# Optimization experiments

Measured on AMD Instinct MI355X. Metric: run time of the kernel, lower is better.

## Reference

```python
import jax, jax.numpy as jnp
import numpy as np

D_MODEL = 512
D_STATE = 16
D_CONV = 4
D_INNER = 2 * D_MODEL          # expand = 2 (mamba_ssm default)
DT_RANK = (D_MODEL + 15) // 16  # ceil(d_model/16) = 32
B, L = 2, 2048


def setup_inputs() -> dict:
    key = jax.random.key(0)
    ks = jax.random.split(key, 12)
    s = lambda k, shp, sc: jax.random.normal(k, shp, jnp.float32) * sc
    return {
        "x": s(ks[0], (B, L, D_MODEL), 1.0),
        "context": s(ks[1], (B, L, D_MODEL), 1.0),
        # Mamba params
        "in_proj_w": s(ks[2], (2 * D_INNER, D_MODEL), 0.02),
        "conv_w": s(ks[3], (D_INNER, D_CONV), 0.2),        # depthwise conv kernel
        "conv_b": jnp.zeros((D_INNER,), jnp.float32),
        "x_proj_w": s(ks[4], (DT_RANK + 2 * D_STATE, D_INNER), 0.02),
        "dt_proj_w": s(ks[5], (D_INNER, DT_RANK), 0.1),
        "dt_proj_b": s(ks[6], (D_INNER,), 0.1),
        "A_log": jnp.log(jnp.tile(jnp.arange(1, D_STATE + 1, dtype=jnp.float32), (D_INNER, 1))),
        "D": jnp.ones((D_INNER,), jnp.float32),
        "out_proj_w": s(ks[7], (D_MODEL, D_INNER), 0.02),
        # context gate params
        "gate_w": s(ks[8], (D_MODEL, 2 * D_MODEL), 0.02),
        "gate_b": jnp.zeros((D_MODEL,), jnp.float32),
    }


def _mamba(x, in_proj_w, conv_w, conv_b, x_proj_w, dt_proj_w, dt_proj_b, A_log, D, out_proj_w):
    Bsz, Ln, _ = x.shape
    # input projection -> [B, L, 2*E], split into ssm branch xi and gate z
    xz = jnp.einsum('bld,ed->ble', x, in_proj_w)
    xi, z = jnp.split(xz, 2, axis=-1)
    # causal depthwise conv1d (kernel D_CONV) + SiLU
    xp = jnp.pad(xi, ((0, 0), (D_CONV - 1, 0), (0, 0)))
    xc = sum(xp[:, k:k + Ln, :] * conv_w[:, k] for k in range(D_CONV)) + conv_b
    xc = jax.nn.silu(xc)
    # input-dependent dt, B, C
    dbc = jnp.einsum('ble,fe->blf', xc, x_proj_w)
    dt, Bm, Cm = jnp.split(dbc, [DT_RANK, DT_RANK + D_STATE], axis=-1)
    dt = jax.nn.softplus(jnp.einsum('blr,er->ble', dt, dt_proj_w) + dt_proj_b)  # [B,L,E]
    A = -jnp.exp(A_log)                                   # [E,S]
    dA = jnp.exp(dt[..., None] * A)                       # [B,L,E,S]
    dBx = dt[..., None] * Bm[:, :, None, :] * xc[..., None]  # [B,L,E,S]

    def step(h, ins):
        dA_t, dBx_t, C_t = ins
        h = dA_t * h + dBx_t                              # [B,E,S]
        y = jnp.einsum('bes,bs->be', h, C_t)
        return h, y

    h0 = jnp.zeros((Bsz, D_INNER, D_STATE), x.dtype)
    _, ys = jax.lax.scan(step, h0,
                         (dA.transpose(1, 0, 2, 3), dBx.transpose(1, 0, 2, 3), Cm.transpose(1, 0, 2)))
    y = ys.transpose(1, 0, 2) + xc * D                    # skip term D*x
    y = y * jax.nn.silu(z)                                # gated output
    return jnp.einsum('ble,de->bld', y, out_proj_w)


def reference(x, context, in_proj_w, conv_w, conv_b, x_proj_w, dt_proj_w, dt_proj_b,
              A_log, D, out_proj_w, gate_w, gate_b):
    m = _mamba(x, in_proj_w, conv_w, conv_b, x_proj_w, dt_proj_w, dt_proj_b, A_log, D, out_proj_w)
    g_in = jnp.concatenate([m, context], axis=-1)         # [B,L,2*d_model]
    gate = jax.nn.sigmoid(jnp.einsum('ble,de->bld', g_in, gate_w) + gate_b)
    return m * gate
```

## Files before the change

kernel.cpp:

```cpp
#include <hip/hip_runtime.h>
#include <cstdint>
#include <cstddef>

#define B_SZ   2
#define L_SZ   2048
#define BL     (B_SZ * L_SZ)
#define DMODEL 512
#define DINNER 1024
#define DSTATE 16
#define DTRANK 32
#define DTROWS 16
#define NCH    32
#define CHL    (L_SZ / NCH)

typedef unsigned short u16;
typedef __attribute__((ext_vector_type(8))) short          bf16x8;
typedef __attribute__((ext_vector_type(8))) unsigned short u16x8;
typedef __attribute__((ext_vector_type(4))) float          f32x4;

__device__ __forceinline__ void gload16(const void* g, void* l) {
    __builtin_amdgcn_global_load_lds(
        (const __attribute__((address_space(1))) unsigned int*)g,
        (__attribute__((address_space(3))) unsigned int*)l, 16, 0, 0);
}

__device__ __forceinline__ u16 bf16_rne(float x) {
    unsigned u = __float_as_uint(x);
    return (u16)((u + 0x7fffu + ((u >> 16) & 1u)) >> 16);
}

__global__ __launch_bounds__(256) void cvt_hl_k(
    const float* __restrict__ src, u16* __restrict__ hi, u16* __restrict__ lo,
    int shift, int dst_stride, int col_off)
{
    const long long base = ((long long)blockIdx.x * 256 + threadIdx.x) * 8;
    const long long row  = base >> shift;
    const int       col  = (int)(base & ((1 << shift) - 1));
    float4 f0 = *(const float4*)(src + base);
    float4 f1 = *(const float4*)(src + base + 4);
    float f[8] = {f0.x, f0.y, f0.z, f0.w, f1.x, f1.y, f1.z, f1.w};
    u16x8 h8, l8;
#pragma unroll
    for (int i = 0; i < 8; ++i) {
        u16 hb = bf16_rne(f[i]);
        float hf = __uint_as_float((unsigned)hb << 16);
        h8[i] = hb;
        l8[i] = bf16_rne(f[i] - hf);
    }
    const long long d = row * dst_stride + col_off + col;
    *(u16x8*)(hi + d) = h8;
    *(u16x8*)(lo + d) = l8;
}

template<int NF, int EPI>
__global__ __launch_bounds__(256) void gemm_bf16hl(
    const u16* __restrict__ Ah, const u16* __restrict__ Al,
    const u16* __restrict__ Wh, const u16* __restrict__ Wl,
    const float* __restrict__ bias, const float* __restrict__ Mul,
    float* __restrict__ C, float* __restrict__ C2, int M, int N, int K)
{
    constexpr int BN  = NF * 32;
    constexpr int NIB = BN / 16;
    constexpr int TOT = 16 + 2 * NIB;
    __shared__ u16 sAh[128][32], sAl[128][32];
    __shared__ u16 sBh[BN][32],  sBl[BN][32];

    const int tid  = threadIdx.x;
    const int w    = tid >> 6;
    const int lane = tid & 63;
    const int bm   = blockIdx.x * 128;
    const int bn   = blockIdx.y * BN;
    const int wm   = w >> 1;
    const int wn   = w & 1;
    const int lm   = lane & 15;
    const int lk8  = (lane >> 4) * 8;
    const int srow = lane >> 2;
    const int scol = (lane & 3) * 8;

    f32x4 acc[4][NF];
#pragma unroll
    for (int i = 0; i < 4; ++i)
#pragma unroll
        for (int j = 0; j < NF; ++j) acc[i][j] = (f32x4){0.f, 0.f, 0.f, 0.f};

    for (int k0 = 0; k0 < K; k0 += 32) {
        __syncthreads();
        for (int idx = w; idx < TOT; idx += 4) {
            const u16* gs; u16* ls;
            if (idx < 8)            { gs = Ah + (size_t)(bm + idx * 16 + srow) * K;              ls = &sAh[idx * 16][0]; }
            else if (idx < 16)      { gs = Al + (size_t)(bm + (idx - 8) * 16 + srow) * K;        ls = &sAl[(idx - 8) * 16][0]; }
            else if (idx < 16 + NIB){ gs = Wh + (size_t)(bn + (idx - 16) * 16 + srow) * K;       ls = &sBh[(idx - 16) * 16][0]; }
            else                    { gs = Wl + (size_t)(bn + (idx - 16 - NIB) * 16 + srow) * K; ls = &sBl[(idx - 16 - NIB) * 16][0]; }
            gload16(gs + k0 + scol, ls);
        }
        __syncthreads();

        bf16x8 a_h[4], a_l[4], b_h[NF], b_l[NF];
#pragma unroll
        for (int mi = 0; mi < 4; ++mi) {
            a_h[mi] = *(const bf16x8*)&sAh[wm * 64 + mi * 16 + lm][lk8];
            a_l[mi] = *(const bf16x8*)&sAl[wm * 64 + mi * 16 + lm][lk8];
        }
#pragma unroll
        for (int ni = 0; ni < NF; ++ni) {
            b_h[ni] = *(const bf16x8*)&sBh[wn * (NF * 16) + ni * 16 + lm][lk8];
            b_l[ni] = *(const bf16x8*)&sBl[wn * (NF * 16) + ni * 16 + lm][lk8];
        }
#pragma unroll
        for (int mi = 0; mi < 4; ++mi)
#pragma unroll
            for (int ni = 0; ni < NF; ++ni) {
                acc[mi][ni] = __builtin_amdgcn_mfma_f32_16x16x32_bf16(a_h[mi], b_h[ni], acc[mi][ni], 0, 0, 0);
                acc[mi][ni] = __builtin_amdgcn_mfma_f32_16x16x32_bf16(a_h[mi], b_l[ni], acc[mi][ni], 0, 0, 0);
                acc[mi][ni] = __builtin_amdgcn_mfma_f32_16x16x32_bf16(a_l[mi], b_h[ni], acc[mi][ni], 0, 0, 0);
            }
    }

    const int lr4 = (lane >> 4) * 4;
#pragma unroll
    for (int mi = 0; mi < 4; ++mi)
#pragma unroll
        for (int ni = 0; ni < NF; ++ni)
#pragma unroll
            for (int r = 0; r < 4; ++r) {
                const int row = bm + wm * 64 + mi * 16 + lr4 + r;
                const int col = bn + wn * (NF * 16) + ni * 16 + lm;
                if (EPI == 0) {
                    C[(size_t)row * N + col] = acc[mi][ni][r];
                } else if (EPI == 1) {
                    const size_t o = (size_t)row * N + col;
                    const float v = acc[mi][ni][r] + bias[col];
                    C[o] = Mul[o] / (1.f + expf(-v));
                } else {
                    if (col < DINNER) C [(size_t)row * DINNER + col]          = acc[mi][ni][r];
                    else              C2[(size_t)row * DINNER + col - DINNER] = acc[mi][ni][r];
                }
            }
}

__global__ __launch_bounds__(256) void gemm_xproj(
    const float* __restrict__ A, const float* __restrict__ W,
    float* __restrict__ C, int M, int N, int K)
{
    __shared__ float As[16][64];
    __shared__ float Ws[16][64];
    const int tid  = threadIdx.x;
    const int bm   = blockIdx.x * 64;
    const int tm   = (tid >> 4) * 4;
    const int tn   = (tid & 15) * 4;
    const int lrow = tid >> 2;
    const int lk   = (tid & 3) * 4;

    float acc[4][4];
#pragma unroll
    for (int i = 0; i < 4; ++i)
#pragma unroll
        for (int j = 0; j < 4; ++j) acc[i][j] = 0.f;

    for (int k0 = 0; k0 < K; k0 += 16) {
        const int kk = k0 + lk;
        float4 av = *(const float4*)(A + (size_t)(bm + lrow) * K + kk);
        float4 wv = *(const float4*)(W + (size_t)lrow * K + kk);
        __syncthreads();
        As[lk + 0][lrow] = av.x; As[lk + 1][lrow] = av.y;
        As[lk + 2][lrow] = av.z; As[lk + 3][lrow] = av.w;
        Ws[lk + 0][lrow] = wv.x; Ws[lk + 1][lrow] = wv.y;
        Ws[lk + 2][lrow] = wv.z; Ws[lk + 3][lrow] = wv.w;
        __syncthreads();
#pragma unroll
        for (int k = 0; k < 16; ++k) {
            float4 a4 = *(const float4*)&As[k][tm];
            float4 b4 = *(const float4*)&Ws[k][tn];
            float a[4] = {a4.x, a4.y, a4.z, a4.w};
            float b[4] = {b4.x, b4.y, b4.z, b4.w};
#pragma unroll
            for (int i = 0; i < 4; ++i)
#pragma unroll
                for (int j = 0; j < 4; ++j)
                    acc[i][j] = fmaf(a[i], b[j], acc[i][j]);
        }
    }
#pragma unroll
    for (int i = 0; i < 4; ++i)
        *(float4*)(C + (size_t)(bm + tm + i) * N + tn) =
            make_float4(acc[i][0], acc[i][1], acc[i][2], acc[i][3]);
}

__global__ __launch_bounds__(256) void conv_silu_k(
    const float* __restrict__ xi, const float* __restrict__ cw,
    const float* __restrict__ cb, float* __restrict__ xc)
{
    const int idx = blockIdx.x * 256 + threadIdx.x;
    const int e  = idx & (DINNER - 1);
    const int bl = idx >> 10;
    const int l  = bl & (L_SZ - 1);
    const float4 w = *(const float4*)(cw + e * 4);
    float acc = cb[e];
    acc = fmaf(xi[(size_t)bl * DINNER + e], w.w, acc);
    if (l >= 1) acc = fmaf(xi[(size_t)(bl - 1) * DINNER + e], w.z, acc);
    if (l >= 2) acc = fmaf(xi[(size_t)(bl - 2) * DINNER + e], w.y, acc);
    if (l >= 3) acc = fmaf(xi[(size_t)(bl - 3) * DINNER + e], w.x, acc);
    xc[idx] = acc / (1.f + expf(-acc));
}

__global__ __launch_bounds__(256) void dt_softplus_k(
    const float* __restrict__ dbc, const float* __restrict__ Wdt,
    const float* __restrict__ bdt, float* __restrict__ dt)
{
    __shared__ float r[DTROWS][DTRANK];
    const int rb  = blockIdx.x * DTROWS;
    const int tid = threadIdx.x;
    for (int i = tid; i < DTROWS * DTRANK; i += 256)
        r[i >> 5][i & 31] = dbc[(size_t)(rb + (i >> 5)) * 64 + (i & 31)];
    __syncthreads();
    for (int n = tid; n < DINNER; n += 256) {
        float4 wv[8];
        const float* w = Wdt + (size_t)n * DTRANK;
#pragma unroll
        for (int q = 0; q < 8; ++q) wv[q] = *(const float4*)(w + q * 4);
        const float bn_ = bdt[n];
#pragma unroll
        for (int row = 0; row < DTROWS; ++row) {
            float acc = bn_;
#pragma unroll
            for (int q = 0; q < 8; ++q) {
                acc = fmaf(wv[q].x, r[row][q * 4 + 0], acc);
                acc = fmaf(wv[q].y, r[row][q * 4 + 1], acc);
                acc = fmaf(wv[q].z, r[row][q * 4 + 2], acc);
                acc = fmaf(wv[q].w, r[row][q * 4 + 3], acc);
            }
            dt[(size_t)(rb + row) * DINNER + n] = (acc > 20.f) ? acc : log1pf(expf(acc));
        }
    }
}


__global__ __launch_bounds__(256) void scan_p1(
    const float* __restrict__ dtb, const float* __restrict__ xc,
    const float* __restrict__ dbc, const float* __restrict__ A_log,
    float* __restrict__ Pst, float* __restrict__ Hst)
{
    const int bid = blockIdx.x;
    const int c   = bid & (NCH - 1);
    const int eg  = (bid >> 5) & 7;
    const int b   = bid >> 8;
    const int tid = threadIdx.x;
    const int e    = eg * 128 + (tid >> 1);
    const int s0   = (tid & 1) * 8;

    float A2[8];
    {
        float4 a0 = *(const float4*)(A_log + e * DSTATE + s0);
        float4 a1 = *(const float4*)(A_log + e * DSTATE + s0 + 4);
        const float c2 = 1.44269504088896f;
        A2[0] = -expf(a0.x) * c2; A2[1] = -expf(a0.y) * c2;
        A2[2] = -expf(a0.z) * c2; A2[3] = -expf(a0.w) * c2;
        A2[4] = -expf(a1.x) * c2; A2[5] = -expf(a1.y) * c2;
        A2[6] = -expf(a1.z) * c2; A2[7] = -expf(a1.w) * c2;
    }
    float h[8] = {0.f, 0.f, 0.f, 0.f, 0.f, 0.f, 0.f, 0.f};
    float dtsum = 0.f;
    const size_t base = (size_t)b * L_SZ + (size_t)c * CHL;
    const float* dtp = dtb + base * DINNER + e;
    const float* xcp = xc  + base * DINNER + e;
    const float* dbp = dbc + base * 64 + DTRANK + s0;
    float dtv = *dtp, xcv = *xcp;

    for (int l = 0; l < CHL; ++l) {
        float4 B0 = *(const float4*)(dbp);
        float4 B1 = *(const float4*)(dbp + 4);
        const size_t adv = (l + 1 < CHL) ? DINNER : 0;
        float dt_n = dtp[adv];
        float xc_n = xcp[adv];
        dtsum += dtv;
        const float u = dtv * xcv;
        const float Bs[8] = {B0.x, B0.y, B0.z, B0.w, B1.x, B1.y, B1.z, B1.w};
#pragma unroll
        for (int j = 0; j < 8; ++j) {
            const float dA = exp2f(dtv * A2[j]);
            h[j] = fmaf(dA, h[j], Bs[j] * u);
        }
        dtv = dt_n; xcv = xc_n;
        dtp += DINNER; xcp += DINNER; dbp += 64;
    }
    const size_t off = (((size_t)c * B_SZ + b) * DINNER + e) * DSTATE + s0;
    *(float4*)(Pst + off)     = make_float4(exp2f(A2[0] * dtsum), exp2f(A2[1] * dtsum),
                                            exp2f(A2[2] * dtsum), exp2f(A2[3] * dtsum));
    *(float4*)(Pst + off + 4) = make_float4(exp2f(A2[4] * dtsum), exp2f(A2[5] * dtsum),
                                            exp2f(A2[6] * dtsum), exp2f(A2[7] * dtsum));
    *(float4*)(Hst + off)     = make_float4(h[0], h[1], h[2], h[3]);
    *(float4*)(Hst + off + 4) = make_float4(h[4], h[5], h[6], h[7]);
}

__global__ __launch_bounds__(256) void scan_comb(
    const float* __restrict__ Pst, float* __restrict__ Hst)
{
    const int idx = blockIdx.x * 256 + threadIdx.x;
    float h = 0.f;
    for (int c = 0; c < NCH; ++c) {
        const size_t off = (size_t)c * (B_SZ * DINNER * DSTATE) + idx;
        const float P = Pst[off];
        const float H = Hst[off];
        Hst[off] = h;
        h = fmaf(P, h, H);
    }
}

__global__ __launch_bounds__(256) void scan_p2(
    const float* __restrict__ dtb, const float* __restrict__ xc,
    const float* __restrict__ z, const float* __restrict__ dbc,
    const float* __restrict__ A_log, const float* __restrict__ Dp,
    const float* __restrict__ H0,
    u16* __restrict__ y_hi, u16* __restrict__ y_lo)
{
    const int bid = blockIdx.x;
    const int c   = bid & (NCH - 1);
    const int eg  = (bid >> 5) & 7;
    const int b   = bid >> 8;
    const int tid = threadIdx.x;
    const int e    = eg * 128 + (tid >> 1);
    const int half = tid & 1;
    const int s0   = half * 8;

    float A2[8];
    {
        float4 a0 = *(const float4*)(A_log + e * DSTATE + s0);
        float4 a1 = *(const float4*)(A_log + e * DSTATE + s0 + 4);
        const float c2 = 1.44269504088896f;
        A2[0] = -expf(a0.x) * c2; A2[1] = -expf(a0.y) * c2;
        A2[2] = -expf(a0.z) * c2; A2[3] = -expf(a0.w) * c2;
        A2[4] = -expf(a1.x) * c2; A2[5] = -expf(a1.y) * c2;
        A2[6] = -expf(a1.z) * c2; A2[7] = -expf(a1.w) * c2;
    }
    const float Dv = Dp[e];
    const size_t base = (size_t)b * L_SZ + (size_t)c * CHL;
    const size_t hoff = (((size_t)c * B_SZ + b) * DINNER + e) * DSTATE + s0;
    float h[8];
    {
        float4 h0 = *(const float4*)(H0 + hoff);
        float4 h1 = *(const float4*)(H0 + hoff + 4);
        h[0] = h0.x; h[1] = h0.y; h[2] = h0.z; h[3] = h0.w;
        h[4] = h1.x; h[5] = h1.y; h[6] = h1.z; h[7] = h1.w;
    }
    const float* dtp = dtb + base * DINNER + e;
    const float* xcp = xc  + base * DINNER + e;
    const float* zp  = z   + base * DINNER + e;
    const float* dbp = dbc + base * 64 + DTRANK + s0;
    float dtv = *dtp, xcv = *xcp, zv = *zp;

    for (int l = 0; l < CHL; ++l) {
        float4 B0 = *(const float4*)(dbp);
        float4 B1 = *(const float4*)(dbp + 4);
        float4 C0 = *(const float4*)(dbp + DSTATE);
        float4 C1 = *(const float4*)(dbp + DSTATE + 4);
        const size_t adv = (l + 1 < CHL) ? DINNER : 0;
        float dt_n = dtp[adv];
        float xc_n = xcp[adv];
        float z_n  = zp[adv];
        const float u = dtv * xcv;
        const float Bs[8] = {B0.x, B0.y, B0.z, B0.w, B1.x, B1.y, B1.z, B1.w};
        const float Cs[8] = {C0.x, C0.y, C0.z, C0.w, C1.x, C1.y, C1.z, C1.w};
        float yp = 0.f;
#pragma unroll
        for (int j = 0; j < 8; ++j) {
            const float dA = exp2f(dtv * A2[j]);
            h[j] = fmaf(dA, h[j], Bs[j] * u);
            yp = fmaf(h[j], Cs[j], yp);
        }
        yp += __shfl_xor(yp, 1);
        const float sg = zv / (1.f + expf(-zv));
        const float yv = fmaf(xcv, Dv, yp) * sg;
        const u16 hb = bf16_rne(yv);
        const size_t o = (base + l) * DINNER + e;
        if (half == 0) y_hi[o] = hb;
        else           y_lo[o] = bf16_rne(yv - __uint_as_float((unsigned)hb << 16));
        dtv = dt_n; xcv = xc_n; zv = z_n;
        dtp += DINNER; xcp += DINNER; zp += DINNER; dbp += 64;
    }
}

extern "C" void kernel_launch(void* const* d_in, const int* in_sizes, int n_in,
                              void* d_out, int out_size, void* d_ws, size_t ws_size,
                              hipStream_t stream)
{
    const float* x         = (const float*)d_in[0];
    const float* context   = (const float*)d_in[1];
    const float* in_proj_w = (const float*)d_in[2];
    const float* conv_w    = (const float*)d_in[3];
    const float* conv_b    = (const float*)d_in[4];
    const float* x_proj_w  = (const float*)d_in[5];
    const float* dt_proj_w = (const float*)d_in[6];
    const float* dt_proj_b = (const float*)d_in[7];
    const float* A_log     = (const float*)d_in[8];
    const float* Dvec      = (const float*)d_in[9];
    const float* out_proj_w= (const float*)d_in[10];
    const float* gate_w    = (const float*)d_in[11];
    const float* gate_b    = (const float*)d_in[12];
    float* out = (float*)d_out;

    char* wsb = (char*)d_ws;
    float* xi   = (float*)(wsb + (size_t)( 0u << 20));
    float* z    = (float*)(wsb + (size_t)(16u << 20));
    float* xc   = (float*)(wsb + (size_t)(32u << 20));
    float* dbc  = (float*)(wsb + (size_t)(48u << 20));
    float* dt   = (float*)(wsb + (size_t)(49u << 20));
    float* m    = (float*)(wsb + (size_t)(65u << 20));
    u16* x_hi   = (u16*)(wsb + (size_t)(65u << 20));
    u16* x_lo   = (u16*)(wsb + (size_t)(69u << 20));
    float* Pst  = (float*)(wsb + (size_t)(65u << 20));
    float* Hst  = (float*)(wsb + (size_t)(69u << 20));
    u16* Wi_hi  = (u16*)(wsb + (size_t)(73u << 20));
    u16* Wi_lo  = (u16*)(wsb + (size_t)(75u << 20));
    u16* Wo_hi  = (u16*)(wsb + (size_t)(77u << 20));
    u16* Wo_lo  = (u16*)(wsb + (size_t)(78u << 20));
    u16* Wg_hi  = (u16*)(wsb + (size_t)(79u << 20));
    u16* Wg_lo  = (u16*)(wsb + (size_t)(80u << 20));
    u16* y_hi   = (u16*)(wsb + (size_t)( 0u << 20));
    u16* y_lo   = (u16*)(wsb + (size_t)( 8u << 20));
    u16* A7_hi  = (u16*)(wsb + (size_t)(16u << 20));
    u16* A7_lo  = (u16*)(wsb + (size_t)(24u << 20));

    cvt_hl_k<<<1024, 256, 0, stream>>>(x,          x_hi,  x_lo,   9,  512, 0);
    cvt_hl_k<<< 512, 256, 0, stream>>>(in_proj_w,  Wi_hi, Wi_lo,  9,  512, 0);
    cvt_hl_k<<< 256, 256, 0, stream>>>(out_proj_w, Wo_hi, Wo_lo, 10, 1024, 0);
    cvt_hl_k<<< 256, 256, 0, stream>>>(gate_w,     Wg_hi, Wg_lo, 10, 1024, 0);
    gemm_bf16hl<4, 2><<<dim3(BL / 128, 2048 / 128), 256, 0, stream>>>(
        x_hi, x_lo, Wi_hi, Wi_lo, nullptr, nullptr, xi, z, BL, 2048, DMODEL);
    conv_silu_k<<<(BL * DINNER) / 256, 256, 0, stream>>>(xi, conv_w, conv_b, xc);
    gemm_xproj<<<dim3(BL / 64, 1), 256, 0, stream>>>(xc, x_proj_w, dbc, BL, 64, DINNER);
    dt_softplus_k<<<BL / DTROWS, 256, 0, stream>>>(dbc, dt_proj_w, dt_proj_b, dt);
    scan_p1<<<B_SZ * 8 * NCH, 256, 0, stream>>>(dt, xc, dbc, A_log, Pst, Hst);
    scan_comb<<<(B_SZ * DINNER * DSTATE) / 256, 256, 0, stream>>>(Pst, Hst);
    scan_p2<<<B_SZ * 8 * NCH, 256, 0, stream>>>(dt, xc, z, dbc, A_log, Dvec, Hst,
                                                y_hi, y_lo);
    gemm_bf16hl<2, 0><<<dim3(BL / 128, DMODEL / 64), 256, 0, stream>>>(
        y_hi, y_lo, Wo_hi, Wo_lo, nullptr, nullptr, m, nullptr, BL, DMODEL, DINNER);
    cvt_hl_k<<<1024, 256, 0, stream>>>(m,       A7_hi, A7_lo, 9, 1024, 0);
    cvt_hl_k<<<1024, 256, 0, stream>>>(context, A7_hi, A7_lo, 9, 1024, DMODEL);
    gemm_bf16hl<2, 1><<<dim3(BL / 128, DMODEL / 64), 256, 0, stream>>>(
        A7_hi, A7_lo, Wg_hi, Wg_lo, gate_b, m, out, nullptr, BL, DMODEL, 2 * DMODEL);
}
```

Measured before the change: 405.6 us.

## Restructure x_proj GEMM into row-blocked kernel with more blocks

Replaces the 64x64-tiled x_proj GEMM (64 blocks, one per 64 rows, full K loop of 1024) with a kernel where each block stages 8 full rows of xc in LDS and each thread computes two output columns over the whole K. This raises the block count from 64 to 512 so the whole GPU is occupied for this small-N GEMM. Weights are read directly from global memory per thread and rely on cache; per-thread work is a serial 1024-long dot product with a strided, uncoalesced weight access pattern.

```diff
diff --git a/kernel.cpp b/kernel.cpp
--- a/kernel.cpp
+++ b/kernel.cpp
@@ -12,6 +12,7 @@
 #define DTROWS 16
 #define NCH    32
 #define CHL    (L_SZ / NCH)
+#define XPR    8
 
 typedef unsigned short u16;
 typedef __attribute__((ext_vector_type(8))) short          bf16x8;
@@ -140,50 +141,32 @@
 
 __global__ __launch_bounds__(256) void gemm_xproj(
     const float* __restrict__ A, const float* __restrict__ W,
-    float* __restrict__ C, int M, int N, int K)
-{
-    __shared__ float As[16][64];
-    __shared__ float Ws[16][64];
-    const int tid  = threadIdx.x;
-    const int bm   = blockIdx.x * 64;
-    const int tm   = (tid >> 4) * 4;
-    const int tn   = (tid & 15) * 4;
-    const int lrow = tid >> 2;
-    const int lk   = (tid & 3) * 4;
-
-    float acc[4][4];
-#pragma unroll
-    for (int i = 0; i < 4; ++i)
-#pragma unroll
-        for (int j = 0; j < 4; ++j) acc[i][j] = 0.f;
-
-    for (int k0 = 0; k0 < K; k0 += 16) {
-        const int kk = k0 + lk;
-        float4 av = *(const float4*)(A + (size_t)(bm + lrow) * K + kk);
-        float4 wv = *(const float4*)(W + (size_t)lrow * K + kk);
-        __syncthreads();
-        As[lk + 0][lrow] = av.x; As[lk + 1][lrow] = av.y;
-        As[lk + 2][lrow] = av.z; As[lk + 3][lrow] = av.w;
-        Ws[lk + 0][lrow] = wv.x; Ws[lk + 1][lrow] = wv.y;
-        Ws[lk + 2][lrow] = wv.z; Ws[lk + 3][lrow] = wv.w;
-        __syncthreads();
-#pragma unroll
-        for (int k = 0; k < 16; ++k) {
-            float4 a4 = *(const float4*)&As[k][tm];
-            float4 b4 = *(const float4*)&Ws[k][tn];
-            float a[4] = {a4.x, a4.y, a4.z, a4.w};
-            float b[4] = {b4.x, b4.y, b4.z, b4.w};
-#pragma unroll
-            for (int i = 0; i < 4; ++i)
-#pragma unroll
-                for (int j = 0; j < 4; ++j)
-                    acc[i][j] = fmaf(a[i], b[j], acc[i][j]);
-        }
-    }
-#pragma unroll
-    for (int i = 0; i < 4; ++i)
-        *(float4*)(C + (size_t)(bm + tm + i) * N + tn) =
-            make_float4(acc[i][0], acc[i][1], acc[i][2], acc[i][3]);
+    float* __restrict__ C)
+{
+    __shared__ float As[XPR][1028];
+    const int tid = threadIdx.x;
+    const int rb  = blockIdx.x * XPR;
+    for (int i = tid; i < XPR * 256; i += 256) {
+        const int r  = i >> 8;
+        const int k4 = (i & 255) * 4;
+        *(float4*)&As[r][k4] = *(const float4*)(A + (size_t)(rb + r) * DINNER + k4);
+    }
+    __syncthreads();
+    const int r  = tid >> 5;
+    const int c0 = (tid & 31) * 2;
+    const float* w0 = W + (size_t)c0 * DINNER;
+    const float* w1 = w0 + DINNER;
+    float acc0 = 0.f, acc1 = 0.f;
+    for (int k = 0; k < DINNER; k += 4) {
+        const float4 a  = *(const float4*)&As[r][k];
+        const float4 v0 = *(const float4*)(w0 + k);
+        const float4 v1 = *(const float4*)(w1 + k);
+        acc0 = fmaf(a.x, v0.x, acc0); acc0 = fmaf(a.y, v0.y, acc0);
+        acc0 = fmaf(a.z, v0.z, acc0); acc0 = fmaf(a.w, v0.w, acc0);
+        acc1 = fmaf(a.x, v1.x, acc1); acc1 = fmaf(a.y, v1.y, acc1);
+        acc1 = fmaf(a.z, v1.z, acc1); acc1 = fmaf(a.w, v1.w, acc1);
+    }
+    *(float2*)(C + (size_t)(rb + r) * 64 + c0) = make_float2(acc0, acc1);
 }
 
 __global__ __launch_bounds__(256) void conv_silu_k(
@@ -233,7 +216,6 @@
         }
     }
 }
-
 
 __global__ __launch_bounds__(256) void scan_p1(
     const float* __restrict__ dtb, const float* __restrict__ xc,
@@ -427,7 +409,7 @@
     gemm_bf16hl<4, 2><<<dim3(BL / 128, 2048 / 128), 256, 0, stream>>>(
         x_hi, x_lo, Wi_hi, Wi_lo, nullptr, nullptr, xi, z, BL, 2048, DMODEL);
     conv_silu_k<<<(BL * DINNER) / 256, 256, 0, stream>>>(xi, conv_w, conv_b, xc);
-    gemm_xproj<<<dim3(BL / 64, 1), 256, 0, stream>>>(xc, x_proj_w, dbc, BL, 64, DINNER);
+    gemm_xproj<<<BL / XPR, 256, 0, stream>>>(xc, x_proj_w, dbc);
     dt_softplus_k<<<BL / DTROWS, 256, 0, stream>>>(dbc, dt_proj_w, dt_proj_b, dt);
     scan_p1<<<B_SZ * 8 * NCH, 256, 0, stream>>>(dt, xc, dbc, A_log, Pst, Hst);
     scan_comb<<<(B_SZ * DINNER * DSTATE) / 256, 256, 0, stream>>>(Pst, Hst);
```

After: 465.8 us. +14.8%, slower.
